# Kernel optimization log

Measured on AMD Instinct MI355X. Metric: run time of the kernel, lower is better.

The kernel has to match this reference:

```python
import jax, jax.numpy as jnp
import numpy as np

EMBED = 1024
HEADS = 16
HEAD_DIM = EMBED // HEADS


def setup_inputs() -> dict:
    key = jax.random.key(0)
    ks = jax.random.split(key, 11)
    s = 1.0 / np.sqrt(EMBED)
    B, L = 4, 2048
    return {
        "query": jax.random.normal(ks[0], (B, L, EMBED), jnp.float32),
        "key":   jax.random.normal(ks[1], (B, L, EMBED), jnp.float32),
        "value": jax.random.normal(ks[2], (B, L, EMBED), jnp.float32),
        "Wq": jax.random.normal(ks[3], (EMBED, EMBED), jnp.float32) * s,
        "bq": jnp.zeros((EMBED,), jnp.float32),
        "Wk": jax.random.normal(ks[4], (EMBED, EMBED), jnp.float32) * s,
        "bk": jnp.zeros((EMBED,), jnp.float32),
        "Wv": jax.random.normal(ks[5], (EMBED, EMBED), jnp.float32) * s,
        "bv": jnp.zeros((EMBED,), jnp.float32),
        "Wo": jax.random.normal(ks[6], (EMBED, EMBED), jnp.float32) * s,
        "bo": jnp.zeros((EMBED,), jnp.float32),
    }


def reference(query, key, value, Wq, bq, Wk, bk, Wv, bv, Wo, bo):
    N, Lq, E = query.shape
    Lk = key.shape[1]
    # linear projections (torch nn.Linear: x @ W.T + b)
    q = (query @ Wq.T + bq).reshape(N, Lq, HEADS, HEAD_DIM)
    k = (key   @ Wk.T + bk).reshape(N, Lk, HEADS, HEAD_DIM)
    v = (value @ Wv.T + bv).reshape(N, Lk, HEADS, HEAD_DIM)
    # scaled dot-product attention; note: original scales by sqrt(embed_size)
    scale = 1.0 / jnp.sqrt(jnp.float32(E))
    energy = jnp.einsum('nqhd,nkhd->nhqk', q, k) * scale  # [N,H,Lq,Lk]
    score = jax.nn.softmax(energy, axis=-1)
    out = jnp.einsum('nhqk,nkhd->nqhd', score, v).reshape(N, Lq, E)
    return out @ Wo.T + bo
```

## Files before the change

kernel.cpp:

```cpp
#include <hip/hip_runtime.h>
#include <stdint.h>

#define EMBED 1024
#define HEADS 16
#define HDIM 64
#define BATCH 4
#define SEQ 2048
#define ROWS (BATCH*SEQ)
#define QROWS 128

typedef __attribute__((ext_vector_type(8))) __bf16 bf16x8;
typedef __attribute__((ext_vector_type(4))) float f32x4;

#define LDS_U32(p) ((__attribute__((address_space(3))) unsigned int*)(p))
#define GLB_U32(p) ((const __attribute__((address_space(1))) unsigned int*)(p))

__device__ inline unsigned short f2bf(float f) {
    union { float f; unsigned int u; } v; v.f = f;
    unsigned int u = v.u;
    return (unsigned short)((u + 0x7FFFu + ((u >> 16) & 1u)) >> 16);
}

__global__ __launch_bounds__(256) void cvt3(const float* __restrict__ s0, const float* __restrict__ s1,
                                            const float* __restrict__ s2,
                                            unsigned short* __restrict__ d0, unsigned short* __restrict__ d1,
                                            unsigned short* __restrict__ d2) {
    const float* src = (blockIdx.y == 0) ? s0 : (blockIdx.y == 1) ? s1 : s2;
    unsigned short* dst = (blockIdx.y == 0) ? d0 : (blockIdx.y == 1) ? d1 : d2;
    int i = (blockIdx.x * 256 + threadIdx.x) * 4;
    float4 v = *(const float4*)(src + i);
    uint2 p;
    p.x = (unsigned)f2bf(v.x) | ((unsigned)f2bf(v.y) << 16);
    p.y = (unsigned)f2bf(v.z) | ((unsigned)f2bf(v.w) << 16);
    *(uint2*)(dst + i) = p;
}
__global__ __launch_bounds__(256) void cvt4(const float* __restrict__ s0, const float* __restrict__ s1,
                                            const float* __restrict__ s2, const float* __restrict__ s3,
                                            unsigned short* __restrict__ dst, int stride) {
    const float* src = (blockIdx.y == 0) ? s0 : (blockIdx.y == 1) ? s1 : (blockIdx.y == 2) ? s2 : s3;
    unsigned short* d = dst + (size_t)blockIdx.y * stride;
    int i = (blockIdx.x * 256 + threadIdx.x) * 4;
    float4 v = *(const float4*)(src + i);
    uint2 p;
    p.x = (unsigned)f2bf(v.x) | ((unsigned)f2bf(v.y) << 16);
    p.y = (unsigned)f2bf(v.z) | ((unsigned)f2bf(v.w) << 16);
    *(uint2*)(d + i) = p;
}

template <bool OUT_BF16, bool QKV>
__global__ __launch_bounds__(256) void gemm_bt(const unsigned short* __restrict__ A0,
                                               const unsigned short* __restrict__ B0,
                                               const float* __restrict__ bias0,
                                               const float* __restrict__ bias1,
                                               const float* __restrict__ bias2,
                                               void* __restrict__ C0,
                                               unsigned short* __restrict__ vtout,
                                               float scale0,
                                               int M, int N, int K) {
    __shared__ unsigned short As[128 * 64];
    __shared__ unsigned short Bs[128 * 64];

    const int tid  = threadIdx.x;
    const int lane = tid & 63;
    const int wave = tid >> 6;
    const int l15  = lane & 15;
    const int quad = lane >> 4;
    const int wm   = wave & 1;
    const int wn   = wave >> 1;

    const unsigned nx = gridDim.x, ny = gridDim.y;
    const unsigned nwg = nx * ny * gridDim.z;
    const unsigned lin = (blockIdx.z * ny + blockIdx.y) * nx + blockIdx.x;
    const unsigned swz = (lin & 7) * (nwg >> 3) + (lin >> 3);
    const unsigned bx = swz % nx;
    const unsigned rem = swz / nx;
    const unsigned by = rem % ny;
    const unsigned bz = rem / ny;

    const int tileM = by * 128;
    const int tileN = bx * 128;

    const unsigned short* A = A0;
    const unsigned short* B = B0;
    const float* bias = bias0;
    void* C = C0;
    int z = 0;
    float scale = QKV ? scale0 : 1.0f;
    if (QKV) {
        z = bz;
        A = A0 + (size_t)z * M * K;
        B = B0 + (size_t)z * N * K;
        bias = (z == 0) ? bias0 : (z == 1) ? bias1 : bias2;
        C = (void*)((unsigned short*)C0 + (size_t)z * M * N);
        if (z != 0) scale = 1.0f;
    }

    f32x4 acc[4][4] = {};

    for (int k0 = 0; k0 < K; k0 += 64) {
        __syncthreads();
#pragma unroll
        for (int s = 0; s < 4; ++s) {
            int j = tid + s * 256;
            int r = j >> 3;
            int c8 = (j & 7) ^ (r & 7);
            __builtin_amdgcn_global_load_lds(GLB_U32(A + (size_t)(tileM + r) * K + k0 + c8 * 8),
                                             LDS_U32(As + j * 8), 16, 0, 0);
            __builtin_amdgcn_global_load_lds(GLB_U32(B + (size_t)(tileN + r) * K + k0 + c8 * 8),
                                             LDS_U32(Bs + j * 8), 16, 0, 0);
        }
        __syncthreads();

#pragma unroll
        for (int kc = 0; kc < 2; ++kc) {
            bf16x8 a[4], b[4];
#pragma unroll
            for (int i = 0; i < 4; ++i) {
                int ra = wm * 64 + i * 16 + l15;
                a[i] = *(const bf16x8*)(As + ra * 64 + (((kc * 4 + quad) ^ (ra & 7)) * 8));
                int rb = wn * 64 + i * 16 + l15;
                b[i] = *(const bf16x8*)(Bs + rb * 64 + (((kc * 4 + quad) ^ (rb & 7)) * 8));
            }
#pragma unroll
            for (int i = 0; i < 4; ++i)
#pragma unroll
                for (int jn = 0; jn < 4; ++jn)
                    acc[i][jn] = __builtin_amdgcn_mfma_f32_16x16x32_bf16(a[i], b[jn], acc[i][jn], 0, 0, 0);
        }
    }

    if (QKV && z == 2) {
#pragma unroll
        for (int i = 0; i < 4; ++i) {
            int row0 = tileM + wm * 64 + i * 16 + (quad << 2);
            int bb   = row0 >> 11;
            int seq0 = row0 & (SEQ - 1);
#pragma unroll
            for (int jn = 0; jn < 4; ++jn) {
                int col = tileN + wn * 64 + jn * 16 + l15;
                float bv = bias[col];
                uint2 p;
                p.x = (unsigned)f2bf(acc[i][jn][0] + bv) | ((unsigned)f2bf(acc[i][jn][1] + bv) << 16);
                p.y = (unsigned)f2bf(acc[i][jn][2] + bv) | ((unsigned)f2bf(acc[i][jn][3] + bv) << 16);
                *(uint2*)(vtout + ((size_t)(bb * HEADS) * HDIM + col) * SEQ + seq0) = p;
            }
        }
    } else {
#pragma unroll
        for (int i = 0; i < 4; ++i) {
            int row0 = tileM + wm * 64 + i * 16 + (quad << 2);
#pragma unroll
            for (int jn = 0; jn < 4; ++jn) {
                int col = tileN + wn * 64 + jn * 16 + l15;
                float bv = bias[col];
#pragma unroll
                for (int r = 0; r < 4; ++r) {
                    float v = (acc[i][jn][r] + bv) * scale;
                    if (OUT_BF16)
                        ((unsigned short*)C)[(size_t)(row0 + r) * N + col] = f2bf(v);
                    else
                        ((float*)C)[(size_t)(row0 + r) * N + col] = v;
                }
            }
        }
    }
}

__global__ __launch_bounds__(256, 4) void attn(const unsigned short* __restrict__ Q,
                                               const unsigned short* __restrict__ Kp,
                                               const unsigned short* __restrict__ Vt,
                                               unsigned short* __restrict__ O) {
    __shared__ unsigned short KVs[2][2][64 * 64];

    const int tid  = threadIdx.x;
    const int lane = tid & 63;
    const int wave = tid >> 6;
    const int l15  = lane & 15;
    const int quad = lane >> 4;

    const int lin = ((blockIdx.z * HEADS + blockIdx.y) << 4) | blockIdx.x;
    const int swz = ((lin & 7) << 7) | (lin >> 3);
    const int qt = swz & 15;
    const int h  = (swz >> 4) & 15;
    const int b  = swz >> 8;

    const size_t rowbase = (size_t)b * SEQ;
    const int colbase = h * HDIM;
    const size_t vtbase = (size_t)(b * HEADS + h) * HDIM;

#pragma unroll
    for (int s = 0; s < 2; ++s) {
        int j = tid + s * 256;
        int r = j >> 3;
        int sr = (r & 35) | ((r & 12) << 1) | ((r & 16) >> 2);
        int c8 = (j & 7) ^ (r & 7);
        __builtin_amdgcn_global_load_lds(GLB_U32(Kp + (rowbase + sr) * EMBED + colbase + c8 * 8),
                                         LDS_U32(KVs[0][0] + j * 8), 16, 0, 0);
        __builtin_amdgcn_global_load_lds(GLB_U32(Vt + (vtbase + r) * SEQ + c8 * 8),
                                         LDS_U32(KVs[0][1] + j * 8), 16, 0, 0);
    }

    bf16x8 aq[2][2];
#pragma unroll
    for (int mf = 0; mf < 2; ++mf) {
        const unsigned short* qp =
            Q + (rowbase + qt * QROWS + wave * 32 + mf * 16 + l15) * EMBED + colbase;
#pragma unroll
        for (int ks = 0; ks < 2; ++ks)
            aq[mf][ks] = *(const bf16x8*)(qp + ks * 32 + quad * 8);
    }

    const f32x4 fz = {0.0f, 0.0f, 0.0f, 0.0f};
    bf16x8 vone;
#pragma unroll
    for (int i = 0; i < 8; ++i) vone[i] = (__bf16)1.0f;

    f32x4 oacc[2][4] = {};
    f32x4 sumacc[2] = {};

    for (int t = 0; t < 32; ++t) {
        __syncthreads();
        if (t + 1 < 32) {
            int nb = (t + 1) & 1;
#pragma unroll
            for (int s = 0; s < 2; ++s) {
                int j = tid + s * 256;
                int r = j >> 3;
                int sr = (r & 35) | ((r & 12) << 1) | ((r & 16) >> 2);
                int c8 = (j & 7) ^ (r & 7);
                __builtin_amdgcn_global_load_lds(GLB_U32(Kp + (rowbase + (t + 1) * 64 + sr) * EMBED + colbase + c8 * 8),
                                                 LDS_U32(KVs[nb][0] + j * 8), 16, 0, 0);
                __builtin_amdgcn_global_load_lds(GLB_U32(Vt + (vtbase + r) * SEQ + (t + 1) * 64 + c8 * 8),
                                                 LDS_U32(KVs[nb][1] + j * 8), 16, 0, 0);
            }
        }
        const unsigned short* Ks = KVs[t & 1][0];
        const unsigned short* Vs = KVs[t & 1][1];

        f32x4 sacc[2][4];
        __builtin_amdgcn_s_setprio(1);
#pragma unroll
        for (int nf = 0; nf < 4; ++nf) {
            int krow = nf * 16 + l15;
            int ch = quad ^ (krow & 7);
            bf16x8 bk = *(const bf16x8*)(Ks + krow * 64 + ch * 8);
            sacc[0][nf] = __builtin_amdgcn_mfma_f32_16x16x32_bf16(bk, aq[0][0], fz, 0, 0, 0);
            sacc[1][nf] = __builtin_amdgcn_mfma_f32_16x16x32_bf16(bk, aq[1][0], fz, 0, 0, 0);
        }
#pragma unroll
        for (int nf = 0; nf < 4; ++nf) {
            int krow = nf * 16 + l15;
            int ch = (4 + quad) ^ (krow & 7);
            bf16x8 bk = *(const bf16x8*)(Ks + krow * 64 + ch * 8);
            sacc[0][nf] = __builtin_amdgcn_mfma_f32_16x16x32_bf16(bk, aq[0][1], sacc[0][nf], 0, 0, 0);
            sacc[1][nf] = __builtin_amdgcn_mfma_f32_16x16x32_bf16(bk, aq[1][1], sacc[1][nf], 0, 0, 0);
        }
        __builtin_amdgcn_s_setprio(0);

        bf16x8 apv[2][2];
#pragma unroll
        for (int mf = 0; mf < 2; ++mf)
#pragma unroll
            for (int nf = 0; nf < 4; ++nf) {
                int ks2 = nf >> 1;
                int jb = (nf & 1) * 4;
                apv[mf][ks2][jb + 0] = (__bf16)__builtin_amdgcn_exp2f(sacc[mf][nf][0]);
                apv[mf][ks2][jb + 1] = (__bf16)__builtin_amdgcn_exp2f(sacc[mf][nf][1]);
                apv[mf][ks2][jb + 2] = (__bf16)__builtin_amdgcn_exp2f(sacc[mf][nf][2]);
                apv[mf][ks2][jb + 3] = (__bf16)__builtin_amdgcn_exp2f(sacc[mf][nf][3]);
            }

        __builtin_amdgcn_s_setprio(1);
#pragma unroll
        for (int ks = 0; ks < 2; ++ks) {
            sumacc[0] = __builtin_amdgcn_mfma_f32_16x16x32_bf16(apv[0][ks], vone, sumacc[0], 0, 0, 0);
            sumacc[1] = __builtin_amdgcn_mfma_f32_16x16x32_bf16(apv[1][ks], vone, sumacc[1], 0, 0, 0);
#pragma unroll
            for (int df = 0; df < 4; ++df) {
                int vrow = df * 16 + l15;
                int ch = (ks * 4 + quad) ^ (vrow & 7);
                bf16x8 bv = *(const bf16x8*)(Vs + vrow * 64 + ch * 8);
                oacc[0][df] = __builtin_amdgcn_mfma_f32_16x16x32_bf16(apv[0][ks], bv, oacc[0][df], 0, 0, 0);
                oacc[1][df] = __builtin_amdgcn_mfma_f32_16x16x32_bf16(apv[1][ks], bv, oacc[1][df], 0, 0, 0);
            }
        }
        __builtin_amdgcn_s_setprio(0);
    }

    float rinv[2][4];
#pragma unroll
    for (int mf = 0; mf < 2; ++mf)
#pragma unroll
        for (int r = 0; r < 4; ++r)
            rinv[mf][r] = 1.0f / sumacc[mf][r];

#pragma unroll
    for (int mf = 0; mf < 2; ++mf)
#pragma unroll
        for (int df = 0; df < 4; ++df) {
            int col = colbase + df * 16 + l15;
#pragma unroll
            for (int r = 0; r < 4; ++r) {
                int row = qt * QROWS + wave * 32 + mf * 16 + quad * 4 + r;
                O[(rowbase + row) * EMBED + col] = f2bf(oacc[mf][df][r] * rinv[mf][r]);
            }
        }
}

extern "C" void kernel_launch(void* const* d_in, const int* in_sizes, int n_in,
                              void* d_out, int out_size, void* d_ws, size_t ws_size,
                              hipStream_t stream) {
    const float* q_in = (const float*)d_in[0];
    const float* k_in = (const float*)d_in[1];
    const float* v_in = (const float*)d_in[2];
    const float* Wq = (const float*)d_in[3];
    const float* bq = (const float*)d_in[4];
    const float* Wk = (const float*)d_in[5];
    const float* bk = (const float*)d_in[6];
    const float* Wv = (const float*)d_in[7];
    const float* bv = (const float*)d_in[8];
    const float* Wo = (const float*)d_in[9];
    const float* bo = (const float*)d_in[10];
    float* out = (float*)d_out;

    const size_t XE = (size_t)ROWS * EMBED;
    const size_t WE = (size_t)EMBED * EMBED;

    unsigned short* ws = (unsigned short*)d_ws;
    unsigned short* xq = ws;
    unsigned short* xk = xq + XE;
    unsigned short* xv = xk + XE;
    unsigned short* wqkvo = xv + XE;
    unsigned short* wo = wqkvo + 3 * WE;
    unsigned short* Qp = wo + WE;
    unsigned short* Kp = Qp + XE;
    unsigned short* vt = Kp + XE;
    unsigned short* Ap = vt + XE;

    const float cexp = 0.045084436f;

    cvt3<<<dim3((unsigned)(XE / 1024), 3), 256, 0, stream>>>(q_in, k_in, v_in, xq, xk, xv);
    cvt4<<<dim3((unsigned)(WE / 1024), 4), 256, 0, stream>>>(Wq, Wk, Wv, Wo, wqkvo, (int)WE);

    gemm_bt<true, true><<<dim3(EMBED / 128, ROWS / 128, 3), 256, 0, stream>>>(
        xq, wqkvo, bq, bk, bv, Qp, vt, cexp, ROWS, EMBED, EMBED);

    attn<<<dim3(SEQ / QROWS, HEADS, BATCH), 256, 0, stream>>>(Qp, Kp, vt, Ap);

    gemm_bt<false, false><<<dim3(EMBED / 128, ROWS / 128), 256, 0, stream>>>(
        Ap, wo, bo, nullptr, nullptr, out, nullptr, 1.0f, ROWS, EMBED, EMBED);
}
```

Measured before the change: 330.5 us.

## Double-buffer GEMM LDS tiles and merge conversion kernels into one launch

The GEMM now double-buffers its A/B LDS tiles, issuing the next tile's global-to-LDS loads before computing on the current one. It uses a partial vmcnt wait plus raw barriers, so the load latency can overlap with MFMA work. Bias values are hoisted into registers before the main loop. The two fp32-to-bf16 conversion kernels are merged into a single launch to save one kernel dispatch. LDS use per block doubles to 64KB, which may reduce occupancy, and the hand-written waitcnt depends on the compiler emitting exactly 8 loads per stage.

```diff
diff --git a/kernel.cpp b/kernel.cpp
--- a/kernel.cpp
+++ b/kernel.cpp
@@ -21,30 +21,35 @@
     return (unsigned short)((u + 0x7FFFu + ((u >> 16) & 1u)) >> 16);
 }
 
-__global__ __launch_bounds__(256) void cvt3(const float* __restrict__ s0, const float* __restrict__ s1,
-                                            const float* __restrict__ s2,
-                                            unsigned short* __restrict__ d0, unsigned short* __restrict__ d1,
-                                            unsigned short* __restrict__ d2) {
-    const float* src = (blockIdx.y == 0) ? s0 : (blockIdx.y == 1) ? s1 : s2;
-    unsigned short* dst = (blockIdx.y == 0) ? d0 : (blockIdx.y == 1) ? d1 : d2;
-    int i = (blockIdx.x * 256 + threadIdx.x) * 4;
-    float4 v = *(const float4*)(src + i);
+__global__ __launch_bounds__(256) void cvt_all(const float* __restrict__ q, const float* __restrict__ k,
+                                               const float* __restrict__ v,
+                                               const float* __restrict__ wq, const float* __restrict__ wk,
+                                               const float* __restrict__ wv, const float* __restrict__ wo,
+                                               unsigned short* __restrict__ xqkv,
+                                               unsigned short* __restrict__ wqkvo) {
+    const size_t XE = (size_t)ROWS * EMBED;
+    const size_t WE = (size_t)EMBED * EMBED;
+    int g = blockIdx.x;
+    const float* src;
+    unsigned short* dst;
+    size_t off;
+    if (g < 24576) {
+        int arr = g >> 13;
+        src = (arr == 0) ? q : (arr == 1) ? k : v;
+        off = (size_t)(g & 8191) * 1024 + threadIdx.x * 4;
+        dst = xqkv + (size_t)arr * XE;
+    } else {
+        int gw = g - 24576;
+        int arr = gw >> 10;
+        src = (arr == 0) ? wq : (arr == 1) ? wk : (arr == 2) ? wv : wo;
+        off = (size_t)(gw & 1023) * 1024 + threadIdx.x * 4;
+        dst = wqkvo + (size_t)arr * WE;
+    }
+    float4 val = *(const float4*)(src + off);
     uint2 p;
-    p.x = (unsigned)f2bf(v.x) | ((unsigned)f2bf(v.y) << 16);
-    p.y = (unsigned)f2bf(v.z) | ((unsigned)f2bf(v.w) << 16);
-    *(uint2*)(dst + i) = p;
-}
-__global__ __launch_bounds__(256) void cvt4(const float* __restrict__ s0, const float* __restrict__ s1,
-                                            const float* __restrict__ s2, const float* __restrict__ s3,
-                                            unsigned short* __restrict__ dst, int stride) {
-    const float* src = (blockIdx.y == 0) ? s0 : (blockIdx.y == 1) ? s1 : (blockIdx.y == 2) ? s2 : s3;
-    unsigned short* d = dst + (size_t)blockIdx.y * stride;
-    int i = (blockIdx.x * 256 + threadIdx.x) * 4;
-    float4 v = *(const float4*)(src + i);
-    uint2 p;
-    p.x = (unsigned)f2bf(v.x) | ((unsigned)f2bf(v.y) << 16);
-    p.y = (unsigned)f2bf(v.z) | ((unsigned)f2bf(v.w) << 16);
-    *(uint2*)(d + i) = p;
+    p.x = (unsigned)f2bf(val.x) | ((unsigned)f2bf(val.y) << 16);
+    p.y = (unsigned)f2bf(val.z) | ((unsigned)f2bf(val.w) << 16);
+    *(uint2*)(dst + off) = p;
 }
 
 template <bool OUT_BF16, bool QKV>
@@ -57,8 +62,8 @@
                                                unsigned short* __restrict__ vtout,
                                                float scale0,
                                                int M, int N, int K) {
-    __shared__ unsigned short As[128 * 64];
-    __shared__ unsigned short Bs[128 * 64];
+    __shared__ unsigned short As[2][128 * 64];
+    __shared__ unsigned short Bs[2][128 * 64];
 
     const int tid  = threadIdx.x;
     const int lane = tid & 63;
@@ -95,21 +100,45 @@
         if (z != 0) scale = 1.0f;
     }
 
+    float bv4[4];
+#pragma unroll
+    for (int jn = 0; jn < 4; ++jn)
+        bv4[jn] = bias[tileN + wn * 64 + jn * 16 + l15];
+
     f32x4 acc[4][4] = {};
 
-    for (int k0 = 0; k0 < K; k0 += 64) {
-        __syncthreads();
-#pragma unroll
-        for (int s = 0; s < 4; ++s) {
-            int j = tid + s * 256;
-            int r = j >> 3;
-            int c8 = (j & 7) ^ (r & 7);
-            __builtin_amdgcn_global_load_lds(GLB_U32(A + (size_t)(tileM + r) * K + k0 + c8 * 8),
-                                             LDS_U32(As + j * 8), 16, 0, 0);
-            __builtin_amdgcn_global_load_lds(GLB_U32(B + (size_t)(tileN + r) * K + k0 + c8 * 8),
-                                             LDS_U32(Bs + j * 8), 16, 0, 0);
-        }
-        __syncthreads();
+#pragma unroll
+    for (int s = 0; s < 4; ++s) {
+        int j = tid + s * 256;
+        int r = j >> 3;
+        int c8 = (j & 7) ^ (r & 7);
+        __builtin_amdgcn_global_load_lds(GLB_U32(A + (size_t)(tileM + r) * K + c8 * 8),
+                                         LDS_U32(As[0] + j * 8), 16, 0, 0);
+        __builtin_amdgcn_global_load_lds(GLB_U32(B + (size_t)(tileN + r) * K + c8 * 8),
+                                         LDS_U32(Bs[0] + j * 8), 16, 0, 0);
+    }
+
+    const int nt = K >> 6;
+    for (int t = 0; t < nt; ++t) {
+        const int cur = t & 1;
+        if (t + 1 < nt) {
+            const int nb = cur ^ 1;
+            const int k0 = (t + 1) * 64;
+#pragma unroll
+            for (int s = 0; s < 4; ++s) {
+                int j = tid + s * 256;
+                int r = j >> 3;
+                int c8 = (j & 7) ^ (r & 7);
+                __builtin_amdgcn_global_load_lds(GLB_U32(A + (size_t)(tileM + r) * K + k0 + c8 * 8),
+                                                 LDS_U32(As[nb] + j * 8), 16, 0, 0);
+                __builtin_amdgcn_global_load_lds(GLB_U32(B + (size_t)(tileN + r) * K + k0 + c8 * 8),
+                                                 LDS_U32(Bs[nb] + j * 8), 16, 0, 0);
+            }
+            asm volatile("s_waitcnt vmcnt(8)" ::: "memory");
+        } else {
+            asm volatile("s_waitcnt vmcnt(0)" ::: "memory");
+        }
+        __builtin_amdgcn_s_barrier();
 
 #pragma unroll
         for (int kc = 0; kc < 2; ++kc) {
@@ -117,9 +146,9 @@
 #pragma unroll
             for (int i = 0; i < 4; ++i) {
                 int ra = wm * 64 + i * 16 + l15;
-                a[i] = *(const bf16x8*)(As + ra * 64 + (((kc * 4 + quad) ^ (ra & 7)) * 8));
+                a[i] = *(const bf16x8*)(As[cur] + ra * 64 + (((kc * 4 + quad) ^ (ra & 7)) * 8));
                 int rb = wn * 64 + i * 16 + l15;
-                b[i] = *(const bf16x8*)(Bs + rb * 64 + (((kc * 4 + quad) ^ (rb & 7)) * 8));
+                b[i] = *(const bf16x8*)(Bs[cur] + rb * 64 + (((kc * 4 + quad) ^ (rb & 7)) * 8));
             }
 #pragma unroll
             for (int i = 0; i < 4; ++i)
@@ -127,6 +156,7 @@
                 for (int jn = 0; jn < 4; ++jn)
                     acc[i][jn] = __builtin_amdgcn_mfma_f32_16x16x32_bf16(a[i], b[jn], acc[i][jn], 0, 0, 0);
         }
+        __builtin_amdgcn_s_barrier();
     }
 
     if (QKV && z == 2) {
@@ -138,7 +168,7 @@
 #pragma unroll
             for (int jn = 0; jn < 4; ++jn) {
                 int col = tileN + wn * 64 + jn * 16 + l15;
-                float bv = bias[col];
+                float bv = bv4[jn];
                 uint2 p;
                 p.x = (unsigned)f2bf(acc[i][jn][0] + bv) | ((unsigned)f2bf(acc[i][jn][1] + bv) << 16);
                 p.y = (unsigned)f2bf(acc[i][jn][2] + bv) | ((unsigned)f2bf(acc[i][jn][3] + bv) << 16);
@@ -152,7 +182,7 @@
 #pragma unroll
             for (int jn = 0; jn < 4; ++jn) {
                 int col = tileN + wn * 64 + jn * 16 + l15;
-                float bv = bias[col];
+                float bv = bv4[jn];
 #pragma unroll
                 for (int r = 0; r < 4; ++r) {
                     float v = (acc[i][jn][r] + bv) * scale;
@@ -328,9 +358,7 @@
 
     unsigned short* ws = (unsigned short*)d_ws;
     unsigned short* xq = ws;
-    unsigned short* xk = xq + XE;
-    unsigned short* xv = xk + XE;
-    unsigned short* wqkvo = xv + XE;
+    unsigned short* wqkvo = xq + 3 * XE;
     unsigned short* wo = wqkvo + 3 * WE;
     unsigned short* Qp = wo + WE;
     unsigned short* Kp = Qp + XE;
@@ -339,8 +367,7 @@
 
     const float cexp = 0.045084436f;
 
-    cvt3<<<dim3((unsigned)(XE / 1024), 3), 256, 0, stream>>>(q_in, k_in, v_in, xq, xk, xv);
-    cvt4<<<dim3((unsigned)(WE / 1024), 4), 256, 0, stream>>>(Wq, Wk, Wv, Wo, wqkvo, (int)WE);
+    cvt_all<<<dim3(28672), 256, 0, stream>>>(q_in, k_in, v_in, Wq, Wk, Wv, Wo, xq, wqkvo);
 
     gemm_bt<true, true><<<dim3(EMBED / 128, ROWS / 128, 3), 256, 0, stream>>>(
         xq, wqkvo, bq, bk, bv, Qp, vt, cexp, ROWS, EMBED, EMBED);
```

New measurement: 320.6 us. 1.03x faster.
